# Performance work log

Measured on AMD Instinct MI355X. Metric: run time of the kernel, lower is better.

The kernel has to match this reference:

```python
import jax, jax.numpy as jnp
import numpy as np

H, D, E, C, F = 12, 64, 768, 512, 3072  # heads, kq_dim, emb_dim, context_dim, mlp_hid
EPS = 1e-5
SCALE = 1.0 / float(np.sqrt(D))


def setup_inputs() -> dict:
    key = jax.random.key(0)
    ks = jax.random.split(key, 12)
    rn = lambda k, s: jax.random.normal(k, s, dtype=jnp.float32) * 0.02
    z = lambda s: jnp.zeros(s, jnp.float32)
    o = lambda s: jnp.ones(s, jnp.float32)
    return {
        "emb": jax.random.normal(ks[0], (8, 1024, E), dtype=jnp.float32),
        "context": jax.random.normal(ks[1], (8, 256, C), dtype=jnp.float32),
        # self-attention (qkv_bias=False, value_up has bias)
        "sa_wq": rn(ks[2], (E, H * D)), "sa_wk": rn(ks[3], (E, H * D)),
        "sa_wv": rn(ks[4], (E, H * D)), "sa_wo": rn(ks[5], (H * D, E)), "sa_wo_b": z((E,)),
        "sa_qn_g": o((D,)), "sa_qn_b": z((D,)), "sa_kn_g": o((D,)), "sa_kn_b": z((D,)),
        # cross-attention
        "ca_wq": rn(ks[6], (E, H * D)), "ca_wk": rn(ks[7], (C, H * D)),
        "ca_wv": rn(ks[8], (C, H * D)), "ca_wo": rn(ks[9], (H * D, E)), "ca_wo_b": z((E,)),
        "ca_qn_g": o((D,)), "ca_qn_b": z((D,)), "ca_kn_g": o((D,)), "ca_kn_b": z((D,)),
        # MLP
        "mlp_w1": rn(ks[10], (E, F)), "mlp_b1": z((F,)),
        "mlp_w2": rn(ks[11], (F, E)), "mlp_b2": z((E,)),
        # block LayerNorms
        "ln1_g": o((E,)), "ln1_b": z((E,)),
        "ln2_g": o((E,)), "ln2_b": z((E,)),
        "ln3_g": o((E,)), "ln3_b": z((E,)),
    }


def _ln(x, g, b):
    m = jnp.mean(x, axis=-1, keepdims=True)
    v = jnp.mean(jnp.square(x - m), axis=-1, keepdims=True)
    return (x - m) / jnp.sqrt(v + EPS) * g + b


def _heads(x):  # [B,S,H*D] -> [B,H,S,D]
    B, S = x.shape[:2]
    return x.reshape(B, S, H, D).transpose(0, 2, 1, 3)


def _merge(x):  # [B,H,S,D] -> [B,S,H*D]
    B, h, S, d = x.shape
    return x.transpose(0, 2, 1, 3).reshape(B, S, h * d)


def _attn(qx, kvx, wq, wk, wv, wo, wo_b, qg, qb, kg, kb):
    q = _ln(_heads(qx @ wq), qg, qb)   # per-head QK-LayerNorm
    k = _ln(_heads(kvx @ wk), kg, kb)
    v = _heads(kvx @ wv)
    a = jax.nn.softmax(jnp.einsum('bhqd,bhkd->bhqk', q, k) * SCALE, axis=-1)
    return _merge(jnp.einsum('bhqk,bhkd->bhqd', a, v)) @ wo + wo_b


def reference(emb, context,
              sa_wq, sa_wk, sa_wv, sa_wo, sa_wo_b, sa_qn_g, sa_qn_b, sa_kn_g, sa_kn_b,
              ca_wq, ca_wk, ca_wv, ca_wo, ca_wo_b, ca_qn_g, ca_qn_b, ca_kn_g, ca_kn_b,
              mlp_w1, mlp_b1, mlp_w2, mlp_b2,
              ln1_g, ln1_b, ln2_g, ln2_b, ln3_g, ln3_b):
    # MultiHeadAttention.forward returns value + emb, and the block adds emb again
    sa = _attn(emb, emb, sa_wq, sa_wk, sa_wv, sa_wo, sa_wo_b,
               sa_qn_g, sa_qn_b, sa_kn_g, sa_kn_b)
    x = _ln(sa + emb + emb, ln1_g, ln1_b)  # faithful double residual
    ca = _attn(x, context, ca_wq, ca_wk, ca_wv, ca_wo, ca_wo_b,
               ca_qn_g, ca_qn_b, ca_kn_g, ca_kn_b)
    x = _ln(x + ca, ln2_g, ln2_b)
    x = jax.nn.gelu(x @ mlp_w1 + mlp_b1, approximate=False) @ mlp_w2 + mlp_b2
    return _ln(x, ln3_g, ln3_b)  # note: no residual around MLP in the original
```

## Files before the change

kernel.cpp:

```cpp
#include <hip/hip_runtime.h>
#include <hip/hip_bf16.h>
#include <math.h>

#define NH 12
#define HD 64
#define ED 768
#define CD 512
#define FD 3072
#define BB 8
#define SS 1024
#define TT 256
#define LN_EPS 1e-5f
#define ATT_SCALE 0.125f
#define QSC_LOG2E 0.1803368801111204f
#define P_M0 11.55f
#define TOT_R 6291456

typedef __attribute__((ext_vector_type(8))) __bf16 bf16x8;
typedef __attribute__((ext_vector_type(4))) __bf16 bf16x4;
typedef __attribute__((ext_vector_type(4))) float f32x4;

typedef const __attribute__((address_space(1))) void* gas1_t;
typedef __attribute__((address_space(3))) void* las3_t;

__device__ __forceinline__ void gl16(const void* g, void* l) {
  __builtin_amdgcn_global_load_lds((gas1_t)g, (las3_t)l, 16, 0, 0);
}

__device__ __forceinline__ ushort f2bf(float f) {
  union { __bf16 b; ushort u; } c;
  c.b = (__bf16)f;
  return c.u;
}

__device__ __forceinline__ bf16x8 frag64(const ushort (*T)[64], int row, int q8) {
  return *(const bf16x8*)((const char*)T + row * 128 + ((q8 ^ (row & 7)) << 4));
}

struct CvtPack {
  const float* src[12];
  ushort* dst[12];
  int kd[12];
  int nd[12];
  int off[13];
};

__global__ __launch_bounds__(256) void cvt_all(CvtPack P) {
  __shared__ float t[32][33];
  const int flat = blockIdx.x;
  int j = 0;
  while (j < 11 && flat >= P.off[j + 1]) ++j;
  const int rel = flat - P.off[j];
  if (P.nd[j] == 0) {
    const int i = rel * 256 + threadIdx.x;
    if (i < P.kd[j]) {
      float4 v = ((const float4*)P.src[j])[i];
      ((ushort4*)P.dst[j])[i] =
          make_ushort4(f2bf(v.x), f2bf(v.y), f2bf(v.z), f2bf(v.w));
    }
    return;
  }
  const int Kd = P.kd[j], Nd = P.nd[j];
  const int ntx = Nd >> 5;
  const int n0 = (rel % ntx) * 32, k0 = (rel / ntx) * 32;
  const float* W = P.src[j];
  ushort* WT = P.dst[j];
  const int tx = threadIdx.x & 31, ty = threadIdx.x >> 5;
#pragma unroll
  for (int r = 0; r < 4; ++r)
    t[ty + 8 * r][tx] = W[(size_t)(k0 + ty + 8 * r) * Nd + n0 + tx];
  __syncthreads();
#pragma unroll
  for (int r = 0; r < 4; ++r)
    WT[(size_t)(n0 + ty + 8 * r) * Kd + k0 + tx] = f2bf(t[tx][ty + 8 * r]);
}

template <int MODE>
__global__ __launch_bounds__(256) void mfma_gemm(
    const ushort* __restrict__ A, const ushort* __restrict__ Wt,
    const float* __restrict__ bias, void* __restrict__ outp,
    int M, int N, int K, int sshift,
    const float* __restrict__ qg, const float* __restrict__ qb,
    const float* __restrict__ kg, const float* __restrict__ kb,
    int t_q, int t_k, int t_v) {
  __shared__ ushort As[128][64];
  __shared__ ushort Bs[128][64];
  const int tid = threadIdx.x;
  const int m0 = blockIdx.x * 128, n0 = blockIdx.y * 128;
  const int lane = tid & 63;
  const int wr = ((tid >> 6) >> 1) * 64, wc = ((tid >> 6) & 1) * 64;
  const int l15 = lane & 15, g = lane >> 4;
  f32x4 acc[4][4] = {};

  for (int kt = 0; kt < K; kt += 64) {
    __syncthreads();
#pragma unroll
    for (int p = 0; p < 4; ++p) {
      const int flat = p * 256 + tid;
      const int row = flat >> 3, q8 = flat & 7;
      const int kc = 8 * (q8 ^ (row & 7));
      gl16(&A[(size_t)(m0 + row) * K + kt + kc], (char*)As + flat * 16);
      gl16(&Wt[(size_t)(n0 + row) * K + kt + kc], (char*)Bs + flat * 16);
    }
    __syncthreads();
#pragma unroll
    for (int h = 0; h < 2; ++h) {
      bf16x8 af[4], bfv[4];
#pragma unroll
      for (int i = 0; i < 4; ++i) {
        af[i] = frag64(As, wr + i * 16 + l15, 4 * h + g);
        bfv[i] = frag64(Bs, wc + i * 16 + l15, 4 * h + g);
      }
#pragma unroll
      for (int i = 0; i < 4; ++i)
#pragma unroll
        for (int j = 0; j < 4; ++j)
          acc[i][j] = __builtin_amdgcn_mfma_f32_16x16x32_bf16(af[i], bfv[j],
                                                              acc[i][j], 0, 0, 0);
    }
  }

  if (MODE == 2) {
    ushort* out = (ushort*)outp;
    const int Stok = 1 << sshift, smask = Stok - 1;
    const int ht0 = (n0 + wc) >> 6;
    const int t = ht0 / NH, h = ht0 - t * NH;
    const bool isq = (t == t_q), isk = (t == t_k);
    if (isq || isk) {
      const float* gg = isq ? qg : kg;
      const float* bb = isq ? qb : kb;
      const float osc = isq ? QSC_LOG2E : 1.0f;
      float gv[4], bv[4];
#pragma unroll
      for (int j = 0; j < 4; ++j) {
        gv[j] = gg[j * 16 + l15];
        bv[j] = bb[j * 16 + l15];
      }
#pragma unroll
      for (int i = 0; i < 4; ++i)
#pragma unroll
        for (int r = 0; r < 4; ++r) {
          float s = acc[i][0][r] + acc[i][1][r] + acc[i][2][r] + acc[i][3][r];
          float sq = acc[i][0][r] * acc[i][0][r] + acc[i][1][r] * acc[i][1][r] +
                     acc[i][2][r] * acc[i][2][r] + acc[i][3][r] * acc[i][3][r];
          s += __shfl_xor(s, 1);  sq += __shfl_xor(sq, 1);
          s += __shfl_xor(s, 2);  sq += __shfl_xor(sq, 2);
          s += __shfl_xor(s, 4);  sq += __shfl_xor(sq, 4);
          s += __shfl_xor(s, 8);  sq += __shfl_xor(sq, 8);
          const float mean = s * (1.0f / 64.0f);
          const float var = sq * (1.0f / 64.0f) - mean * mean;
          const float rs = rsqrtf(fmaxf(var, 0.0f) + LN_EPS);
#pragma unroll
          for (int j = 0; j < 4; ++j)
            acc[i][j][r] = ((acc[i][j][r] - mean) * rs * gv[j] + bv[j]) * osc;
        }
    }
    if (t == t_v) {
#pragma unroll
      for (int i = 0; i < 4; ++i) {
        const int row = m0 + wr + i * 16 + g * 4;
        const int b = row >> sshift, s2 = row & smask;
        ushort* obase =
            out + (size_t)t * TOT_R + (((size_t)b * NH + h) * 64) * Stok + s2;
#pragma unroll
        for (int j = 0; j < 4; ++j) {
          const int d = j * 16 + l15;
          ushort4 pk = make_ushort4(f2bf(acc[i][j][0]), f2bf(acc[i][j][1]),
                                    f2bf(acc[i][j][2]), f2bf(acc[i][j][3]));
          *(ushort4*)&obase[(size_t)d * Stok] = pk;
        }
      }
    } else {
#pragma unroll
      for (int i = 0; i < 4; ++i)
#pragma unroll
        for (int r = 0; r < 4; ++r) {
          const int row = m0 + wr + i * 16 + g * 4 + r;
          const int b = row >> sshift, s2 = row & smask;
          ushort* orow =
              out + (size_t)t * TOT_R + (((size_t)b * NH + h) * Stok + s2) * 64;
#pragma unroll
          for (int j = 0; j < 4; ++j) orow[j * 16 + l15] = f2bf(acc[i][j][r]);
        }
    }
  } else {
#pragma unroll
    for (int i = 0; i < 4; ++i) {
#pragma unroll
      for (int j = 0; j < 4; ++j) {
        const int gc = n0 + wc + j * 16 + l15;
        const float bv = bias ? bias[gc] : 0.0f;
#pragma unroll
        for (int r = 0; r < 4; ++r) {
          const int row = m0 + wr + i * 16 + g * 4 + r;
          float c = acc[i][j][r] + bv;
          if (MODE == 1) {
            c = 0.5f * c * (1.0f + erff(c * 0.70710678118654752f));
            ((ushort*)outp)[(size_t)row * N + gc] = f2bf(c);
          } else {
            ((float*)outp)[(size_t)row * N + gc] = c;
          }
        }
      }
    }
  }
}

__global__ __launch_bounds__(512) void flash_mfma(
    const ushort* __restrict__ Q, const ushort* __restrict__ K,
    const ushort* __restrict__ V, ushort* __restrict__ out, int Tkv) {
  __shared__ ushort Ks[2][64][64];
  __shared__ ushort Vt[2][80][64];
  __shared__ ushort Ps[8][16][64];
  const int bh = blockIdx.x;
  const int b = bh / NH, h = bh % NH;
  const int qt = blockIdx.y;
  const int tid = threadIdx.x;
  const int w = tid >> 6, lane = tid & 63;
  const int l15 = lane & 15, g = lane >> 4;
  const int srow = tid >> 3;
  const int q8s = tid & 7;
  const int skc = 8 * (q8s ^ (srow & 7));
  const int kperm = 4 * (srow & 15) + (srow >> 4);

  const ushort* Qb = Q + ((size_t)bh * SS + qt * 256) * 64;
  const ushort* Kb = K + (size_t)bh * Tkv * 64;
  const ushort* Vb = V + (size_t)bh * Tkv * 64;

  gl16(&Kb[(size_t)kperm * 64 + skc], (char*)Ks[0] + tid * 16);
  gl16(&Vb[(size_t)srow * Tkv + skc], (char*)Vt[0] + tid * 16);

  if (tid < 256) {
    const int bi = tid >> 7, rq = tid & 127;
    const uint4 ov = make_uint4(0x3F803F80u, 0x3F803F80u, 0x3F803F80u, 0x3F803F80u);
    *(uint4*)((char*)Vt[bi] + (64 + (rq >> 3)) * 128 + ((rq & 7) << 4)) = ov;
  }

  const ushort* qr0 = Qb + (w * 32 + l15) * 64;
  const bf16x8 qf00 = *(const bf16x8*)&qr0[g * 8];
  const bf16x8 qf01 = *(const bf16x8*)&qr0[32 + g * 8];
  const bf16x8 qf10 = *(const bf16x8*)&qr0[16 * 64 + g * 8];
  const bf16x8 qf11 = *(const bf16x8*)&qr0[16 * 64 + 32 + g * 8];
  __syncthreads();

  f32x4 oa[2][5] = {};
  const int pwofs = ((((l15 >> 1) ^ ((g * 4) & 7)) << 4) | ((l15 & 1) << 3));

  const int nch = Tkv >> 6;
  int cur = 0;
  for (int ci = 0; ci < nch; ++ci) {
    if (ci + 1 < nch) {
      const int cnx = (ci + 1) << 6;
      const int nxt = cur ^ 1;
      gl16(&Kb[(size_t)(cnx + kperm) * 64 + skc], (char*)Ks[nxt] + tid * 16);
      gl16(&Vb[(size_t)srow * Tkv + cnx + skc], (char*)Vt[nxt] + tid * 16);
    }

    f32x4 s[2][4] = {};
    __builtin_amdgcn_s_setprio(1);
#pragma unroll
    for (int kb = 0; kb < 4; ++kb) {
      bf16x8 kf0 = frag64(Ks[cur], kb * 16 + l15, g);
      bf16x8 kf1 = frag64(Ks[cur], kb * 16 + l15, 4 + g);
      s[0][kb] = __builtin_amdgcn_mfma_f32_16x16x32_bf16(qf00, kf0, s[0][kb], 0, 0, 0);
      s[0][kb] = __builtin_amdgcn_mfma_f32_16x16x32_bf16(qf01, kf1, s[0][kb], 0, 0, 0);
      s[1][kb] = __builtin_amdgcn_mfma_f32_16x16x32_bf16(qf10, kf0, s[1][kb], 0, 0, 0);
      s[1][kb] = __builtin_amdgcn_mfma_f32_16x16x32_bf16(qf11, kf1, s[1][kb], 0, 0, 0);
    }
    __builtin_amdgcn_s_setprio(0);

    bf16x8 pfr[2][2];
#pragma unroll
    for (int sub = 0; sub < 2; ++sub) {
#pragma unroll
      for (int r = 0; r < 4; ++r) {
        bf16x4 pk;
#pragma unroll
        for (int kbv = 0; kbv < 4; ++kbv)
          pk[kbv] = (__bf16)exp2f(s[sub][kbv][r] - P_M0);
        *(bf16x4*)((char*)Ps[w] + (g * 4 + r) * 128 + (pwofs ^ ((r & 7) << 4))) = pk;
      }
      pfr[sub][0] = frag64(Ps[w], l15, g);
      pfr[sub][1] = frag64(Ps[w], l15, 4 + g);
    }

    __builtin_amdgcn_s_setprio(1);
#pragma unroll
    for (int jd = 0; jd < 5; ++jd) {
      const int d = jd * 16 + l15;
      bf16x8 vf0 = frag64(Vt[cur], d, g);
      bf16x8 vf1 = frag64(Vt[cur], d, 4 + g);
      oa[0][jd] = __builtin_amdgcn_mfma_f32_16x16x32_bf16(pfr[0][0], vf0, oa[0][jd], 0, 0, 0);
      oa[0][jd] = __builtin_amdgcn_mfma_f32_16x16x32_bf16(pfr[0][1], vf1, oa[0][jd], 0, 0, 0);
      oa[1][jd] = __builtin_amdgcn_mfma_f32_16x16x32_bf16(pfr[1][0], vf0, oa[1][jd], 0, 0, 0);
      oa[1][jd] = __builtin_amdgcn_mfma_f32_16x16x32_bf16(pfr[1][1], vf1, oa[1][jd], 0, 0, 0);
    }
    __builtin_amdgcn_s_setprio(0);

    __syncthreads();
    cur ^= 1;
  }

#pragma unroll
  for (int sub = 0; sub < 2; ++sub)
#pragma unroll
    for (int r = 0; r < 4; ++r) {
      const int row = qt * 256 + w * 32 + sub * 16 + g * 4 + r;
      const float inv = 1.0f / oa[sub][4][r];
#pragma unroll
      for (int jd = 0; jd < 4; ++jd)
        out[((size_t)b * SS + row) * ED + h * 64 + jd * 16 + l15] =
            f2bf(oa[sub][jd][r] * inv);
    }
}

__global__ __launch_bounds__(256) void add_ln(
    const float* __restrict__ a, const float* __restrict__ bsrc, float alpha,
    const float* __restrict__ g, const float* __restrict__ bt,
    float* __restrict__ outf, ushort* __restrict__ outb) {
  const int row = blockIdx.x;
  const int tid = threadIdx.x;
  const size_t base = (size_t)row * ED;
  float x[3];
#pragma unroll
  for (int k = 0; k < 3; ++k) {
    int idx = tid + k * 256;
    float v = a[base + idx];
    if (bsrc) v += alpha * bsrc[base + idx];
    x[k] = v;
  }
  float s = x[0] + x[1] + x[2];
  for (int off = 32; off; off >>= 1) s += __shfl_xor(s, off);
  __shared__ float red[4];
  __shared__ float red2[4];
  if ((tid & 63) == 0) red[tid >> 6] = s;
  __syncthreads();
  float mean = (red[0] + red[1] + red[2] + red[3]) * (1.0f / 768.0f);
  float v = 0.f;
#pragma unroll
  for (int k = 0; k < 3; ++k) {
    float t = x[k] - mean;
    v += t * t;
  }
  for (int off = 32; off; off >>= 1) v += __shfl_xor(v, off);
  if ((tid & 63) == 0) red2[tid >> 6] = v;
  __syncthreads();
  float var = (red2[0] + red2[1] + red2[2] + red2[3]) * (1.0f / 768.0f);
  float rs = rsqrtf(var + LN_EPS);
#pragma unroll
  for (int k = 0; k < 3; ++k) {
    int idx = tid + k * 256;
    float y = (x[k] - mean) * rs * g[idx] + bt[idx];
    if (outf) outf[base + idx] = y;
    if (outb) outb[base + idx] = f2bf(y);
  }
}

extern "C" void kernel_launch(void* const* d_in, const int* in_sizes, int n_in,
                              void* d_out, int out_size, void* d_ws,
                              size_t ws_size, hipStream_t stream) {
  (void)in_sizes; (void)n_in; (void)out_size; (void)ws_size;
  const float* emb     = (const float*)d_in[0];
  const float* context = (const float*)d_in[1];
  const float* sa_wq = (const float*)d_in[2];
  const float* sa_wk = (const float*)d_in[3];
  const float* sa_wv = (const float*)d_in[4];
  const float* sa_wo = (const float*)d_in[5];
  const float* sa_wo_b = (const float*)d_in[6];
  const float* sa_qn_g = (const float*)d_in[7];
  const float* sa_qn_b = (const float*)d_in[8];
  const float* sa_kn_g = (const float*)d_in[9];
  const float* sa_kn_b = (const float*)d_in[10];
  const float* ca_wq = (const float*)d_in[11];
  const float* ca_wk = (const float*)d_in[12];
  const float* ca_wv = (const float*)d_in[13];
  const float* ca_wo = (const float*)d_in[14];
  const float* ca_wo_b = (const float*)d_in[15];
  const float* ca_qn_g = (const float*)d_in[16];
  const float* ca_qn_b = (const float*)d_in[17];
  const float* ca_kn_g = (const float*)d_in[18];
  const float* ca_kn_b = (const float*)d_in[19];
  const float* mlp_w1 = (const float*)d_in[20];
  const float* mlp_b1 = (const float*)d_in[21];
  const float* mlp_w2 = (const float*)d_in[22];
  const float* mlp_b2 = (const float*)d_in[23];
  const float* ln1_g = (const float*)d_in[24];
  const float* ln1_b = (const float*)d_in[25];
  const float* ln2_g = (const float*)d_in[26];
  const float* ln2_b = (const float*)d_in[27];
  const float* ln3_g = (const float*)d_in[28];
  const float* ln3_b = (const float*)d_in[29];
  float* out = (float*)d_out;

  const size_t R = TOT_R;
  ushort* U = (ushort*)d_ws;
  ushort* Qh  = U;
  ushort* Kh  = U + R;
  ushort* Vh  = U + 2 * R;
  ushort* SH1 = U + 3 * R;
  ushort* SH2 = U + 4 * R;
  ushort* WB  = U + 5 * R;
  float*  X1  = (float*)(U + 5 * R + 9043968);
  float*  WOt = (float*)Qh;
  ushort* Hb  = Qh;

  ushort* w_saqkv = WB;
  ushort* w_sao   = WB + 1769472;
  ushort* w_caq   = WB + 2359296;
  ushort* w_cakv  = WB + 2949120;
  ushort* w_cao   = WB + 3735552;
  ushort* w_m1    = WB + 4325376;
  ushort* w_m2    = WB + 6684672;

  dim3 blk(256);

  CvtPack P;
  const float* srcs[12] = {sa_wq, sa_wk, sa_wv, sa_wo, ca_wq, ca_wk, ca_wv,
                           ca_wo, mlp_w1, mlp_w2, emb, context};
  ushort* dsts[12] = {w_saqkv, w_saqkv + 589824, w_saqkv + 1179648, w_sao,
                      w_caq, w_cakv, w_cakv + 393216, w_cao, w_m1, w_m2,
                      SH1, SH2};
  const int kds[12] = {ED, ED, ED, ED, ED, CD, CD, ED, ED, FD,
                       1572864, 262144};
  const int nds[12] = {ED, ED, ED, ED, ED, ED, ED, ED, FD, ED, 0, 0};
  int off = 0;
  for (int j = 0; j < 12; ++j) {
    P.src[j] = srcs[j]; P.dst[j] = dsts[j]; P.kd[j] = kds[j]; P.nd[j] = nds[j];
    P.off[j] = off;
    off += nds[j] ? (nds[j] >> 5) * (kds[j] >> 5) : (kds[j] + 255) >> 8;
  }
  P.off[12] = off;
  cvt_all<<<dim3(off), blk, 0, stream>>>(P);

  mfma_gemm<2><<<dim3(64, 18), blk, 0, stream>>>(
      SH1, w_saqkv, nullptr, Qh, 8192, 2304, ED, 10,
      sa_qn_g, sa_qn_b, sa_kn_g, sa_kn_b, 0, 1, 2);
  flash_mfma<<<dim3(96, 4), dim3(512), 0, stream>>>(Qh, Kh, Vh, SH1, SS);
  mfma_gemm<0><<<dim3(64, 6), blk, 0, stream>>>(
      SH1, w_sao, sa_wo_b, X1, 8192, ED, ED, 0,
      nullptr, nullptr, nullptr, nullptr, -1, -1, -1);
  add_ln<<<dim3(8192), blk, 0, stream>>>(X1, emb, 2.0f, ln1_g, ln1_b, X1, SH1);

  mfma_gemm<2><<<dim3(64, 6), blk, 0, stream>>>(
      SH1, w_caq, nullptr, Qh, 8192, ED, ED, 10,
      ca_qn_g, ca_qn_b, nullptr, nullptr, 0, -1, -1);
  mfma_gemm<2><<<dim3(16, 12), blk, 0, stream>>>(
      SH2, w_cakv, nullptr, Kh, 2048, 1536, CD, 8,
      nullptr, nullptr, ca_kn_g, ca_kn_b, -1, 0, 1);
  flash_mfma<<<dim3(96, 4), dim3(512), 0, stream>>>(Qh, Kh, Vh, SH1, TT);
  mfma_gemm<0><<<dim3(64, 6), blk, 0, stream>>>(
      SH1, w_cao, ca_wo_b, WOt, 8192, ED, ED, 0,
      nullptr, nullptr, nullptr, nullptr, -1, -1, -1);
  add_ln<<<dim3(8192), blk, 0, stream>>>(WOt, X1, 1.0f, ln2_g, ln2_b, nullptr, SH2);

  mfma_gemm<1><<<dim3(64, 24), blk, 0, stream>>>(
      SH2, w_m1, mlp_b1, Hb, 8192, FD, ED, 0,
      nullptr, nullptr, nullptr, nullptr, -1, -1, -1);
  mfma_gemm<0><<<dim3(64, 6), blk, 0, stream>>>(
      Hb, w_m2, mlp_b2, X1, 8192, ED, FD, 0,
      nullptr, nullptr, nullptr, nullptr, -1, -1, -1);
  add_ln<<<dim3(8192), blk, 0, stream>>>(X1, nullptr, 0.0f, ln3_g, ln3_b, out,
                                         nullptr);
}
```

Before: 393.0 us.

## Double-buffer GEMM tiles, use fast GELU/exp2, and wave-per-row LayerNorm

The GEMM kernel now uses double-buffered LDS tiles: it prefetches the next K tile while running MFMAs on the current one, and needs one barrier per iteration instead of two. The exact erf GELU is replaced by a sigmoid-form tanh approximation built on hardware exp2 and rcp, and the attention softmax also calls the hardware exp2 intrinsic. LayerNorm now processes one row per wave with float4 loads and no shared-memory reductions, launched with 4 rows per block. These changes trade some GELU accuracy and double the GEMM LDS footprint for reduced memory stalls and cheaper math.

```diff
diff --git a/kernel.cpp b/kernel.cpp
--- a/kernel.cpp
+++ b/kernel.cpp
@@ -33,6 +33,12 @@
   return c.u;
 }
 
+__device__ __forceinline__ float gelu_fast(float c) {
+  const float x2 = c * c;
+  const float ex = __builtin_amdgcn_exp2f(c * (-2.3022084f - 0.10294325f * x2));
+  return c * __builtin_amdgcn_rcpf(1.0f + ex);
+}
+
 __device__ __forceinline__ bf16x8 frag64(const ushort (*T)[64], int row, int q8) {
   return *(const bf16x8*)((const char*)T + row * 128 + ((q8 ^ (row & 7)) << 4));
 }
@@ -83,8 +89,8 @@
     const float* __restrict__ qg, const float* __restrict__ qb,
     const float* __restrict__ kg, const float* __restrict__ kb,
     int t_q, int t_k, int t_v) {
-  __shared__ ushort As[128][64];
-  __shared__ ushort Bs[128][64];
+  __shared__ ushort As[2][128][64];
+  __shared__ ushort Bs[2][128][64];
   const int tid = threadIdx.x;
   const int m0 = blockIdx.x * 128, n0 = blockIdx.y * 128;
   const int lane = tid & 63;
@@ -92,24 +98,29 @@
   const int l15 = lane & 15, g = lane >> 4;
   f32x4 acc[4][4] = {};
 
-  for (int kt = 0; kt < K; kt += 64) {
-    __syncthreads();
+  auto stage = [&](int bi, int kt) {
 #pragma unroll
     for (int p = 0; p < 4; ++p) {
       const int flat = p * 256 + tid;
       const int row = flat >> 3, q8 = flat & 7;
       const int kc = 8 * (q8 ^ (row & 7));
-      gl16(&A[(size_t)(m0 + row) * K + kt + kc], (char*)As + flat * 16);
-      gl16(&Wt[(size_t)(n0 + row) * K + kt + kc], (char*)Bs + flat * 16);
-    }
-    __syncthreads();
+      gl16(&A[(size_t)(m0 + row) * K + kt + kc], (char*)As[bi] + flat * 16);
+      gl16(&Wt[(size_t)(n0 + row) * K + kt + kc], (char*)Bs[bi] + flat * 16);
+    }
+  };
+
+  stage(0, 0);
+  __syncthreads();
+  int cur = 0;
+  for (int kt = 0; kt < K; kt += 64) {
+    if (kt + 64 < K) stage(cur ^ 1, kt + 64);
 #pragma unroll
     for (int h = 0; h < 2; ++h) {
       bf16x8 af[4], bfv[4];
 #pragma unroll
       for (int i = 0; i < 4; ++i) {
-        af[i] = frag64(As, wr + i * 16 + l15, 4 * h + g);
-        bfv[i] = frag64(Bs, wc + i * 16 + l15, 4 * h + g);
+        af[i] = frag64(As[cur], wr + i * 16 + l15, 4 * h + g);
+        bfv[i] = frag64(Bs[cur], wc + i * 16 + l15, 4 * h + g);
       }
 #pragma unroll
       for (int i = 0; i < 4; ++i)
@@ -118,6 +129,8 @@
           acc[i][j] = __builtin_amdgcn_mfma_f32_16x16x32_bf16(af[i], bfv[j],
                                                               acc[i][j], 0, 0, 0);
     }
+    __syncthreads();
+    cur ^= 1;
   }
 
   if (MODE == 2) {
@@ -195,7 +208,7 @@
           const int row = m0 + wr + i * 16 + g * 4 + r;
           float c = acc[i][j][r] + bv;
           if (MODE == 1) {
-            c = 0.5f * c * (1.0f + erff(c * 0.70710678118654752f));
+            c = gelu_fast(c);
             ((ushort*)outp)[(size_t)row * N + gc] = f2bf(c);
           } else {
             ((float*)outp)[(size_t)row * N + gc] = c;
@@ -277,7 +290,7 @@
         bf16x4 pk;
 #pragma unroll
         for (int kbv = 0; kbv < 4; ++kbv)
-          pk[kbv] = (__bf16)exp2f(s[sub][kbv][r] - P_M0);
+          pk[kbv] = (__bf16)__builtin_amdgcn_exp2f(s[sub][kbv][r] - P_M0);
         *(bf16x4*)((char*)Ps[w] + (g * 4 + r) * 128 + (pwofs ^ ((r & 7) << 4))) = pk;
       }
       pfr[sub][0] = frag64(Ps[w], l15, g);
@@ -318,41 +331,49 @@
     const float* __restrict__ a, const float* __restrict__ bsrc, float alpha,
     const float* __restrict__ g, const float* __restrict__ bt,
     float* __restrict__ outf, ushort* __restrict__ outb) {
-  const int row = blockIdx.x;
-  const int tid = threadIdx.x;
+  const int row = blockIdx.x * 4 + (threadIdx.x >> 6);
+  const int lane = threadIdx.x & 63;
   const size_t base = (size_t)row * ED;
-  float x[3];
-#pragma unroll
-  for (int k = 0; k < 3; ++k) {
-    int idx = tid + k * 256;
-    float v = a[base + idx];
-    if (bsrc) v += alpha * bsrc[base + idx];
-    x[k] = v;
-  }
-  float s = x[0] + x[1] + x[2];
+  float4 x[3];
+#pragma unroll
+  for (int p = 0; p < 3; ++p) {
+    const int idx = p * 256 + lane * 4;
+    x[p] = *(const float4*)&a[base + idx];
+    if (bsrc) {
+      float4 bv = *(const float4*)&bsrc[base + idx];
+      x[p].x += alpha * bv.x;
+      x[p].y += alpha * bv.y;
+      x[p].z += alpha * bv.z;
+      x[p].w += alpha * bv.w;
+    }
+  }
+  float s = 0.f;
+#pragma unroll
+  for (int p = 0; p < 3; ++p) s += x[p].x + x[p].y + x[p].z + x[p].w;
   for (int off = 32; off; off >>= 1) s += __shfl_xor(s, off);
-  __shared__ float red[4];
-  __shared__ float red2[4];
-  if ((tid & 63) == 0) red[tid >> 6] = s;
-  __syncthreads();
-  float mean = (red[0] + red[1] + red[2] + red[3]) * (1.0f / 768.0f);
+  const float mean = s * (1.0f / 768.0f);
   float v = 0.f;
 #pragma unroll
-  for (int k = 0; k < 3; ++k) {
-    float t = x[k] - mean;
-    v += t * t;
+  for (int p = 0; p < 3; ++p) {
+    float d0 = x[p].x - mean, d1 = x[p].y - mean;
+    float d2 = x[p].z - mean, d3 = x[p].w - mean;
+    v += d0 * d0 + d1 * d1 + d2 * d2 + d3 * d3;
   }
   for (int off = 32; off; off >>= 1) v += __shfl_xor(v, off);
-  if ((tid & 63) == 0) red2[tid >> 6] = v;
-  __syncthreads();
-  float var = (red2[0] + red2[1] + red2[2] + red2[3]) * (1.0f / 768.0f);
-  float rs = rsqrtf(var + LN_EPS);
-#pragma unroll
-  for (int k = 0; k < 3; ++k) {
-    int idx = tid + k * 256;
-    float y = (x[k] - mean) * rs * g[idx] + bt[idx];
-    if (outf) outf[base + idx] = y;
-    if (outb) outb[base + idx] = f2bf(y);
+  const float rs = rsqrtf(v * (1.0f / 768.0f) + LN_EPS);
+#pragma unroll
+  for (int p = 0; p < 3; ++p) {
+    const int idx = p * 256 + lane * 4;
+    const float4 gv = *(const float4*)&g[idx];
+    const float4 bb = *(const float4*)&bt[idx];
+    const float y0 = (x[p].x - mean) * rs * gv.x + bb.x;
+    const float y1 = (x[p].y - mean) * rs * gv.y + bb.y;
+    const float y2 = (x[p].z - mean) * rs * gv.z + bb.z;
+    const float y3 = (x[p].w - mean) * rs * gv.w + bb.w;
+    if (outf) *(float4*)&outf[base + idx] = make_float4(y0, y1, y2, y3);
+    if (outb)
+      *(ushort4*)&outb[base + idx] =
+          make_ushort4(f2bf(y0), f2bf(y1), f2bf(y2), f2bf(y3));
   }
 }
 
@@ -439,7 +460,7 @@
   mfma_gemm<0><<<dim3(64, 6), blk, 0, stream>>>(
       SH1, w_sao, sa_wo_b, X1, 8192, ED, ED, 0,
       nullptr, nullptr, nullptr, nullptr, -1, -1, -1);
-  add_ln<<<dim3(8192), blk, 0, stream>>>(X1, emb, 2.0f, ln1_g, ln1_b, X1, SH1);
+  add_ln<<<dim3(2048), blk, 0, stream>>>(X1, emb, 2.0f, ln1_g, ln1_b, X1, SH1);
 
   mfma_gemm<2><<<dim3(64, 6), blk, 0, stream>>>(
       SH1, w_caq, nullptr, Qh, 8192, ED, ED, 10,
@@ -451,7 +472,7 @@
   mfma_gemm<0><<<dim3(64, 6), blk, 0, stream>>>(
       SH1, w_cao, ca_wo_b, WOt, 8192, ED, ED, 0,
       nullptr, nullptr, nullptr, nullptr, -1, -1, -1);
-  add_ln<<<dim3(8192), blk, 0, stream>>>(WOt, X1, 1.0f, ln2_g, ln2_b, nullptr, SH2);
+  add_ln<<<dim3(2048), blk, 0, stream>>>(WOt, X1, 1.0f, ln2_g, ln2_b, nullptr, SH2);
 
   mfma_gemm<1><<<dim3(64, 24), blk, 0, stream>>>(
       SH2, w_m1, mlp_b1, Hb, 8192, FD, ED, 0,
@@ -459,6 +480,6 @@
   mfma_gemm<0><<<dim3(64, 6), blk, 0, stream>>>(
       Hb, w_m2, mlp_b2, X1, 8192, ED, FD, 0,
       nullptr, nullptr, nullptr, nullptr, -1, -1, -1);
-  add_ln<<<dim3(8192), blk, 0, stream>>>(X1, nullptr, 0.0f, ln3_g, ln3_b, out,
+  add_ln<<<dim3(2048), blk, 0, stream>>>(X1, nullptr, 0.0f, ln3_g, ln3_b, out,
                                          nullptr);
 }
```

Result: faster. 342.5 us (median of 2 runs) (-12.8%).
